# Optimization experiments

Measured on AMD Instinct MI355X. Metric: run time of the kernel, lower is better.

Reference implementation:

```python
import jax, jax.numpy as jnp
import numpy as np

# E2M1 FP4 value table: codes 0-7 positive, 8-15 negative (sign bit = MSB)
FP4_LUT = jnp.array([0.0, 0.5, 1.0, 1.5, 2.0, 3.0, 4.0, 6.0,
                     -0.0, -0.5, -1.0, -1.5, -2.0, -3.0, -4.0, -6.0],
                    dtype=jnp.float32)
GROUP = 32  # MX microscaling block size


def _dequant(codes, scales):
    # codes: [O, I] int in [0,16); scales: [O, I//GROUP] power-of-two floats
    vals = FP4_LUT[codes]                          # [O, I]
    return vals * jnp.repeat(scales, GROUP, axis=1)  # broadcast group scale


def setup_inputs() -> dict:
    key = jax.random.key(0)
    ks = jax.random.split(key, 7)
    T, D, G = 8192, 4096, GROUP
    x = jax.random.normal(ks[0], (T, D), dtype=jnp.float32)
    w1_codes = jax.random.randint(ks[1], (D, D), 0, 16, dtype=jnp.int32)
    w1_scales = (2.0 ** jax.random.randint(ks[2], (D, D // G), -6, 2)).astype(jnp.float32)
    b1 = jax.random.normal(ks[3], (D,), dtype=jnp.float32) * 0.01
    w2_codes = jax.random.randint(ks[4], (D, D), 0, 16, dtype=jnp.int32)
    w2_scales = (2.0 ** jax.random.randint(ks[5], (D, D // G), -6, 2)).astype(jnp.float32)
    b2 = jax.random.normal(ks[6], (D,), dtype=jnp.float32) * 0.01
    return {"x": x, "w1_codes": w1_codes, "w1_scales": w1_scales, "b1": b1,
            "w2_codes": w2_codes, "w2_scales": w2_scales, "b2": b2}


def reference(x, w1_codes, w1_scales, b1, w2_codes, w2_scales, b2):
    # first MXFP4 quant linear: y = x @ dequant(W1)^T + b1
    h = x @ _dequant(w1_codes, w1_scales).T + b1
    # second MXFP4 quant linear
    y = h @ _dequant(w2_codes, w2_scales).T + b2
    return y
```

## Files before the change

### kernel.cpp

```cpp
#include <hip/hip_runtime.h>


typedef __bf16 bf16;
typedef bf16 bf16x8 __attribute__((ext_vector_type(8)));
typedef float f32x4 __attribute__((ext_vector_type(4)));
typedef int intx4 __attribute__((ext_vector_type(4)));

#define T_DIM 8192
#define D_DIM 4096

__device__ __forceinline__ void gld_lds16(const void* g, void* l) {
    __builtin_amdgcn_global_load_lds(
        (const __attribute__((address_space(1))) void*)g,
        (__attribute__((address_space(3))) void*)l,
        16, 0, 0);
}

__global__ __launch_bounds__(256) void dequant_kernel(
    const int* __restrict__ codes, const float* __restrict__ scales,
    bf16* __restrict__ out)
{
    const size_t tid = (size_t)blockIdx.x * 256 + threadIdx.x;
    const size_t e = tid * 8;
    const int row = (int)(e >> 12);
    const int col = (int)(e & 4095);
    const float s = scales[(size_t)row * (D_DIM / 32) + (col >> 5)];
    const intx4 c0 = *(const intx4*)(codes + e);
    const intx4 c1 = *(const intx4*)(codes + e + 4);
    bf16x8 o;
#pragma unroll
    for (int i = 0; i < 8; ++i) {
        const int c = (i < 4) ? c0[i] : c1[i - 4];
        float v = (float)((0xC8643210u >> ((c & 7) * 4)) & 0xF) * 0.5f;
        v = (c & 8) ? -v : v;
        o[i] = (bf16)(v * s);
    }
    *(bf16x8*)(out + e) = o;
}

__global__ __launch_bounds__(256) void f32_to_bf16_kernel(
    const float* __restrict__ in, bf16* __restrict__ out)
{
    const size_t tid = (size_t)blockIdx.x * 256 + threadIdx.x;
    const size_t e = tid * 8;
    const float4 a = *(const float4*)(in + e);
    const float4 b = *(const float4*)(in + e + 4);
    bf16x8 o;
    o[0] = (bf16)a.x; o[1] = (bf16)a.y; o[2] = (bf16)a.z; o[3] = (bf16)a.w;
    o[4] = (bf16)b.x; o[5] = (bf16)b.y; o[6] = (bf16)b.z; o[7] = (bf16)b.w;
    *(bf16x8*)(out + e) = o;
}

template <bool OUT_BF16>
__global__ __launch_bounds__(256, 2) void gemm_bt_kernel(
    const bf16* __restrict__ A, const bf16* __restrict__ B,
    const float* __restrict__ bias, void* __restrict__ Cout,
    int M, int N, int K)
{
    __shared__ bf16 As[128 * 32];
    __shared__ bf16 Bs[128 * 32];

    const int t = threadIdx.x;
    const int wave = t >> 6;
    const int lane = t & 63;
    const int m0 = blockIdx.y * 128;
    const int n0 = blockIdx.x * 128;
    const int wm = (wave & 1) * 64;
    const int wn = (wave >> 1) * 64;

    f32x4 acc[4][4] = {};

    const int off0 = t * 16;
    const int row0 = off0 >> 6, colb0 = off0 & 63;
    const int off1 = 4096 + t * 16;
    const int row1 = off1 >> 6, colb1 = off1 & 63;
    const int ldsbase = (t & 0xC0) * 16;

    const bf16* pa0 = A + (size_t)(m0 + row0) * K + (colb0 >> 1);
    const bf16* pa1 = A + (size_t)(m0 + row1) * K + (colb1 >> 1);
    const bf16* pb0 = B + (size_t)(n0 + row0) * K + (colb0 >> 1);
    const bf16* pb1 = B + (size_t)(n0 + row1) * K + (colb1 >> 1);

    const int fr = lane & 15;
    const int quad = lane >> 4;

    for (int k0 = 0; k0 < K; k0 += 32) {
        gld_lds16(pa0 + k0, (char*)As + ldsbase);
        gld_lds16(pa1 + k0, (char*)As + 4096 + ldsbase);
        gld_lds16(pb0 + k0, (char*)Bs + ldsbase);
        gld_lds16(pb1 + k0, (char*)Bs + 4096 + ldsbase);
        __syncthreads();

        bf16x8 af[4], bff[4];
#pragma unroll
        for (int i = 0; i < 4; ++i) {
            af[i]  = *(const bf16x8*)(As + (wm + i * 16 + fr) * 32 + quad * 8);
            bff[i] = *(const bf16x8*)(Bs + (wn + i * 16 + fr) * 32 + quad * 8);
        }
#pragma unroll
        for (int i = 0; i < 4; ++i)
#pragma unroll
            for (int j = 0; j < 4; ++j)
                acc[i][j] = __builtin_amdgcn_mfma_f32_16x16x32_bf16(
                    af[i], bff[j], acc[i][j], 0, 0, 0);
        __syncthreads();
    }

    const int cn = lane & 15;
#pragma unroll
    for (int j = 0; j < 4; ++j) {
        const int gn = n0 + wn + j * 16 + cn;
        const float bv = bias[gn];
#pragma unroll
        for (int i = 0; i < 4; ++i) {
            const int gmBase = m0 + wm + i * 16 + quad * 4;
#pragma unroll
            for (int r = 0; r < 4; ++r) {
                const float v = acc[i][j][r] + bv;
                const size_t idx = (size_t)(gmBase + r) * N + gn;
                if (OUT_BF16) ((bf16*)Cout)[idx] = (bf16)v;
                else          ((float*)Cout)[idx] = v;
            }
        }
    }
}

extern "C" void kernel_launch(void* const* d_in, const int* in_sizes, int n_in,
                              void* d_out, int out_size, void* d_ws, size_t ws_size,
                              hipStream_t stream)
{
    const float* x         = (const float*)d_in[0];
    const int*   w1_codes  = (const int*)d_in[1];
    const float* w1_scales = (const float*)d_in[2];
    const float* b1        = (const float*)d_in[3];
    const int*   w2_codes  = (const int*)d_in[4];
    const float* w2_scales = (const float*)d_in[5];
    const float* b2        = (const float*)d_in[6];
    float* y = (float*)d_out;

    char* ws = (char*)d_ws;
    bf16* Xb = (bf16*)ws;
    bf16* Hb = (bf16*)(ws + (size_t)T_DIM * D_DIM * 2);
    bf16* Wd = (bf16*)(ws + (size_t)2 * T_DIM * D_DIM * 2);

    f32_to_bf16_kernel<<<(T_DIM * (size_t)D_DIM) / 8 / 256, 256, 0, stream>>>(x, Xb);
    dequant_kernel<<<(D_DIM * (size_t)D_DIM) / 8 / 256, 256, 0, stream>>>(w1_codes, w1_scales, Wd);
    dim3 grid(D_DIM / 128, T_DIM / 128);
    gemm_bt_kernel<true><<<grid, 256, 0, stream>>>(Xb, Wd, b1, (void*)Hb,
                                                   T_DIM, D_DIM, D_DIM);
    dequant_kernel<<<(D_DIM * (size_t)D_DIM) / 8 / 256, 256, 0, stream>>>(w2_codes, w2_scales, Wd);
    gemm_bt_kernel<false><<<grid, 256, 0, stream>>>(Hb, Wd, b2, (void*)y,
                                                    T_DIM, D_DIM, D_DIM);
}
```

Measured before the change: 879.2 us.

## Switch GEMM to 32x32x16 MFMA with XOR-swizzled LDS layout

Replaces the 16x16x32 bf16 MFMA tiling (4x4 accumulators per wave) with 32x32x16 MFMA (2x2 accumulators, two k-substeps per 32-wide tile). The global-to-LDS load mapping now XOR-swizzles each row's 16-byte column chunk by the row index, and the fragment reads apply the matching swizzle to cut LDS bank conflicts. The larger MFMA shape needs fewer LDS fragment reads per FLOP. The epilogue is rewritten for the 32x32 accumulator register layout. The kernel is still single-buffered with two barriers per k-step, so load latency stays exposed.

```diff
diff --git a/kernel.cpp b/kernel.cpp
--- a/kernel.cpp
+++ b/kernel.cpp
@@ -3,7 +3,7 @@
 
 typedef __bf16 bf16;
 typedef bf16 bf16x8 __attribute__((ext_vector_type(8)));
-typedef float f32x4 __attribute__((ext_vector_type(4)));
+typedef float f32x16 __attribute__((ext_vector_type(16)));
 typedef int intx4 __attribute__((ext_vector_type(4)));
 
 #define T_DIM 8192
@@ -61,28 +61,27 @@
     __shared__ bf16 Bs[128 * 32];
 
     const int t = threadIdx.x;
+    const int lane = t & 63;
     const int wave = t >> 6;
-    const int lane = t & 63;
     const int m0 = blockIdx.y * 128;
     const int n0 = blockIdx.x * 128;
     const int wm = (wave & 1) * 64;
     const int wn = (wave >> 1) * 64;
 
-    f32x4 acc[4][4] = {};
+    f32x16 acc[2][2] = {};
 
-    const int off0 = t * 16;
-    const int row0 = off0 >> 6, colb0 = off0 & 63;
-    const int off1 = 4096 + t * 16;
-    const int row1 = off1 >> 6, colb1 = off1 & 63;
+    const int r0 = t >> 2;
+    const int c16 = (t & 3) ^ (r0 & 3);
     const int ldsbase = (t & 0xC0) * 16;
 
-    const bf16* pa0 = A + (size_t)(m0 + row0) * K + (colb0 >> 1);
-    const bf16* pa1 = A + (size_t)(m0 + row1) * K + (colb1 >> 1);
-    const bf16* pb0 = B + (size_t)(n0 + row0) * K + (colb0 >> 1);
-    const bf16* pb1 = B + (size_t)(n0 + row1) * K + (colb1 >> 1);
+    const bf16* pa0 = A + (size_t)(m0 + r0) * K + c16 * 8;
+    const bf16* pa1 = A + (size_t)(m0 + r0 + 64) * K + c16 * 8;
+    const bf16* pb0 = B + (size_t)(n0 + r0) * K + c16 * 8;
+    const bf16* pb1 = B + (size_t)(n0 + r0 + 64) * K + c16 * 8;
 
-    const int fr = lane & 15;
-    const int quad = lane >> 4;
+    const int rr = lane & 31;
+    const int hh = lane >> 5;
+    const int sw = lane & 3;
 
     for (int k0 = 0; k0 < K; k0 += 32) {
         gld_lds16(pa0 + k0, (char*)As + ldsbase);
@@ -91,33 +90,38 @@
         gld_lds16(pb1 + k0, (char*)Bs + 4096 + ldsbase);
         __syncthreads();
 
-        bf16x8 af[4], bff[4];
 #pragma unroll
-        for (int i = 0; i < 4; ++i) {
-            af[i]  = *(const bf16x8*)(As + (wm + i * 16 + fr) * 32 + quad * 8);
-            bff[i] = *(const bf16x8*)(Bs + (wn + i * 16 + fr) * 32 + quad * 8);
+        for (int ks = 0; ks < 2; ++ks) {
+            const int scol = ((ks * 2 + hh) ^ sw) * 8;
+            bf16x8 a[2], b[2];
+#pragma unroll
+            for (int i = 0; i < 2; ++i) {
+                a[i] = *(const bf16x8*)(As + (wm + i * 32 + rr) * 32 + scol);
+                b[i] = *(const bf16x8*)(Bs + (wn + i * 32 + rr) * 32 + scol);
+            }
+#pragma unroll
+            for (int i = 0; i < 2; ++i)
+#pragma unroll
+                for (int j = 0; j < 2; ++j)
+                    acc[i][j] = __builtin_amdgcn_mfma_f32_32x32x16_bf16(
+                        a[i], b[j], acc[i][j], 0, 0, 0);
         }
-#pragma unroll
-        for (int i = 0; i < 4; ++i)
-#pragma unroll
-            for (int j = 0; j < 4; ++j)
-                acc[i][j] = __builtin_amdgcn_mfma_f32_16x16x32_bf16(
-                    af[i], bff[j], acc[i][j], 0, 0, 0);
         __syncthreads();
     }
 
-    const int cn = lane & 15;
+    const int cn = lane & 31;
+    const int rbase = 4 * hh;
 #pragma unroll
-    for (int j = 0; j < 4; ++j) {
-        const int gn = n0 + wn + j * 16 + cn;
+    for (int j = 0; j < 2; ++j) {
+        const int gn = n0 + wn + j * 32 + cn;
         const float bv = bias[gn];
 #pragma unroll
-        for (int i = 0; i < 4; ++i) {
-            const int gmBase = m0 + wm + i * 16 + quad * 4;
+        for (int i = 0; i < 2; ++i) {
 #pragma unroll
-            for (int r = 0; r < 4; ++r) {
-                const float v = acc[i][j][r] + bv;
-                const size_t idx = (size_t)(gmBase + r) * N + gn;
+            for (int reg = 0; reg < 16; ++reg) {
+                const int row = (reg & 3) + 8 * (reg >> 2) + rbase;
+                const float v = acc[i][j][reg] + bv;
+                const size_t idx = (size_t)(m0 + wm + i * 32 + row) * N + gn;
                 if (OUT_BF16) ((bf16*)Cout)[idx] = (bf16)v;
                 else          ((float*)Cout)[idx] = v;
             }
```

New measurement: 928.7 us. +5.6%, slower.
